# Optimization experiments

Hardware: AMD Instinct MI355X
Metric: run time of the kernel (lower is better)

## Reference

```python
import jax, jax.numpy as jnp
import numpy as np


def setup_inputs() -> dict:
    key0 = jax.random.key(0)
    kq, kk = jax.random.split(key0)
    # query: small template patch; key: larger reference image to search
    query = jax.random.normal(kq, (4, 1, 48, 48), dtype=jnp.float32)
    key = jax.random.normal(kk, (4, 1, 160, 160), dtype=jnp.float32)
    return {"query": query, "key": key}


def reference(query, key):
    B, C, qh, qw = query.shape
    P = key.shape[3] - qw + 1  # static (shape-derived) Python int

    # im2col: extract all overlapping qh x qw patches from key (stride 1, VALID).
    # Output: [B, C*qh*qw, Ho, Wo] with channel ordering (C, kh, kw) -> matches torch unfold.
    patches = jax.lax.conv_general_dilated_patches(
        key, filter_shape=(qh, qw), window_strides=(1, 1), padding='VALID')
    Ho, Wo = patches.shape[2], patches.shape[3]
    L = Ho * Wo
    patches = patches.reshape(B, C, qh * qw, L)  # [B, C, qh*qw, L]

    # Sort pixel values within each patch (dim 2), and within the query patch.
    sorted_key = jnp.sort(patches, axis=2)                       # [B, C, qh*qw, L]
    sorted_query = jnp.sort(query.reshape(B, C, qh * qw, 1), axis=2)  # [B, C, qh*qw, 1]

    # Mean L1 distance between sorted value distributions, reduced over pixels then channels.
    y = jnp.mean(jnp.abs(sorted_key - sorted_query), axis=2)  # [B, C, L]
    y = jnp.mean(y, axis=1)                                   # [B, L]

    hard_indices = jnp.argmin(y, axis=1)  # [B]
    return hard_indices.reshape(-1), P
```

## Files before the change

kernel.cpp:

```cpp
#include <hip/hip_runtime.h>
#include <stdint.h>

#define B_    4
#define QDIM  48
#define KDIM  160
#define HO    113
#define NQ    (QDIM*QDIM)
#define NB    (KDIM*QDIM)
#define NR    (NB+NQ)
#define T_    1024
#define NW    16
#define NP    10
#define NPAD  10240
#define NCH   10
#define NPAIR 57

#define CIDX16(f) ((f) + ((f) >> 4))

__device__ __forceinline__ uint32_t f2s(float v) {
  uint32_t u = __float_as_uint(v);
  return u ^ ((u & 0x80000000u) ? 0xFFFFFFFFu : 0x80000000u);
}
__device__ __forceinline__ float s2f(uint32_t s) {
  return __uint_as_float(s ^ ((s & 0x80000000u) ? 0x80000000u : 0xFFFFFFFFu));
}

__device__ __forceinline__ int dpp_scan_incl(int v) {
  v += __builtin_amdgcn_update_dpp(0, v, 0x111, 0xF, 0xF, false);
  v += __builtin_amdgcn_update_dpp(0, v, 0x112, 0xF, 0xF, false);
  v += __builtin_amdgcn_update_dpp(0, v, 0x114, 0xF, 0xF, false);
  v += __builtin_amdgcn_update_dpp(0, v, 0x118, 0xF, 0xF, false);
  v += __builtin_amdgcn_update_dpp(0, v, 0x142, 0xA, 0xF, false);
  v += __builtin_amdgcn_update_dpp(0, v, 0x143, 0xC, 0xF, false);
  return v;
}

__global__ void ps_init(unsigned long long* slots) {
  if (threadIdx.x < B_) slots[threadIdx.x] = ~0ULL;
}

__global__ __launch_bounds__(T_, 4)
void ps_band_kernel(const float* __restrict__ query,
                    const float* __restrict__ key,
                    unsigned long long* __restrict__ slots) {
  __shared__ unsigned long long E[NPAD];
  __shared__ uint8_t  pA[NPAD];
  __shared__ uint8_t  pB[NPAD];
  alignas(16) __shared__ uint16_t cnt[17408];
  __shared__ int      waveTot[NW], waveBase[NW];
  __shared__ unsigned long long wbest[NW];

  uint32_t* kA = (uint32_t*)E;
  uint32_t* kB = kA + NPAD;

  const int t    = threadIdx.x;
  const int lane = t & 63;
  const int w    = t >> 6;
  const int b    = blockIdx.x / HO;
  const int oy   = blockIdx.x % HO;
  const float* kp = key   + b * KDIM * KDIM;
  const float* qp = query + b * NQ;

  for (int i = t; i < NPAD; i += T_) {
    uint32_t kk, pp;
    if (i < NB) {
      int r = i / KDIM; int x = i - r * KDIM;
      kk = f2s(kp[(oy + r) * KDIM + x]); pp = (uint32_t)x;
    } else if (i < NR) {
      kk = f2s(qp[i - NB]); pp = 255u;
    } else {
      kk = 0xFFFFFFFFu; pp = 254u;
    }
    kA[i] = kk; pA[i] = (uint8_t)pp;
  }
  __syncthreads();

  const int base = t * NP;

  for (int p = 0; p < 8; ++p) {
    uint32_t* sK = (p & 1) ? kB : kA;
    uint32_t* dK = (p & 1) ? kA : kB;
    uint8_t*  sP = (p & 1) ? pB : pA;
    uint8_t*  dP = (p & 1) ? pA : pB;
    const int sh = p * 4;

    for (int i = t; i < 2176; i += T_) ((uint4*)cnt)[i] = make_uint4(0,0,0,0);
    __syncthreads();

    uint32_t kreg[NP]; uint32_t preg[NP];
    {
      const uint2* kv = reinterpret_cast<const uint2*>(sK + base);
      #pragma unroll
      for (int j = 0; j < 5; ++j) { uint2 q = kv[j]; kreg[2*j] = q.x; kreg[2*j+1] = q.y; }
      const uint16_t* pv = reinterpret_cast<const uint16_t*>(sP + base);
      #pragma unroll
      for (int j = 0; j < 5; ++j) { uint32_t q = pv[j]; preg[2*j] = q & 0xFFu; preg[2*j+1] = q >> 8; }
    }

    #pragma unroll
    for (int j = 0; j < NP; ++j) {
      uint32_t f = CIDX16(((kreg[j] >> sh) & 15u) * T_ + t);
      cnt[f] = (uint16_t)(cnt[f] + 1);
    }
    __syncthreads();

    uint32_t cex[16]; int s = 0;
    #pragma unroll
    for (int j = 0; j < 16; ++j) { int c = cnt[CIDX16(16 * t + j)]; cex[j] = (uint32_t)s; s += c; }

    int incl = dpp_scan_incl(s);
    if (lane == 63) waveTot[w] = incl;
    const int wexcl = incl - s;
    __syncthreads();
    if (t < NW) {
      int v = waveTot[t]; int iw = v;
      #pragma unroll
      for (int d = 1; d < NW; d <<= 1) { int o = __shfl_up(iw, d, NW); if (t >= d) iw += o; }
      waveBase[t] = iw - v;
    }
    __syncthreads();
    const int tb = waveBase[w] + wexcl;
    #pragma unroll
    for (int j = 0; j < 16; ++j) cnt[CIDX16(16 * t + j)] = (uint16_t)(cex[j] + (uint32_t)tb);
    __syncthreads();

    #pragma unroll
    for (int j = 0; j < NP; ++j) {
      uint32_t f = CIDX16(((kreg[j] >> sh) & 15u) * T_ + t);
      uint32_t pos = cnt[f];
      cnt[f] = (uint16_t)(pos + 1);
      dK[pos] = kreg[j];
      dP[pos] = (uint8_t)preg[j];
    }
    __syncthreads();
  }

  {
    uint32_t kk2[NP + 1]; uint32_t pp2[NP];
    {
      const uint2* k2 = reinterpret_cast<const uint2*>(kA + base);
      #pragma unroll
      for (int j = 0; j < 5; ++j) { uint2 q = k2[j]; kk2[2*j] = q.x; kk2[2*j+1] = q.y; }
      kk2[NP] = (t == T_ - 1) ? 0xFFFFFFFFu : kA[base + NP];
      const uint16_t* p2 = reinterpret_cast<const uint16_t*>(pA + base);
      #pragma unroll
      for (int j = 0; j < 5; ++j) { uint32_t q = p2[j]; pp2[2*j] = q & 0xFFu; pp2[2*j+1] = q >> 8; }
    }
    __syncthreads();
    #pragma unroll
    for (int j = 0; j < NP; j += 2) {
      int i = base + j;
      float g0 = (i     < NR - 1) ? s2f(kk2[j + 1]) - s2f(kk2[j])     : 0.0f;
      float g1 = (i + 1 < NR - 1) ? s2f(kk2[j + 2]) - s2f(kk2[j + 1]) : 0.0f;
      int c = i >> 10, e = i & 1023;
      int l = e >> 4, sb = (e >> 1) & 7;
      int pidx = c * 1024 + sb * 128 + l * 2;
      E[pidx]     = (unsigned long long)__float_as_uint(g0) | ((unsigned long long)pp2[j]     << 32);
      E[pidx + 1] = (unsigned long long)__float_as_uint(g1) | ((unsigned long long)pp2[j + 1] << 32);
    }
    __syncthreads();
  }

  unsigned long long mybest = ~0ULL;
  for (int pr = w; pr < NPAIR; pr += NW) {
    const int oxa = 2 * pr, oxb = 2 * pr + 1;
    int carry_a = 0, carry_b = 0;
    float acc_a = 0.f, acc_b = 0.f;
    for (int c = 0; c < NCH; ++c) {
      float ga[16]; int pa_[16], pb_[16];
      int ra = 0, rb = 0;
      const uint4* Ep4 = reinterpret_cast<const uint4*>(E + (c * 1024 + lane * 2));
      #pragma unroll
      for (int sb = 0; sb < 8; ++sb) {
        uint4 e = Ep4[sb * 64];
        {
          uint32_t x = e.y;
          int dq = (x == 255u) ? -1 : 0;
          ra += ((x - (uint32_t)oxa) < (uint32_t)QDIM) ? 1 : dq;
          rb += ((x - (uint32_t)oxb) < (uint32_t)QDIM) ? 1 : dq;
          ga[2 * sb] = __uint_as_float(e.x); pa_[2 * sb] = ra; pb_[2 * sb] = rb;
        }
        {
          uint32_t x = e.w;
          int dq = (x == 255u) ? -1 : 0;
          ra += ((x - (uint32_t)oxa) < (uint32_t)QDIM) ? 1 : dq;
          rb += ((x - (uint32_t)oxb) < (uint32_t)QDIM) ? 1 : dq;
          ga[2 * sb + 1] = __uint_as_float(e.z); pa_[2 * sb + 1] = ra; pb_[2 * sb + 1] = rb;
        }
      }
      const int ia = dpp_scan_incl(ra);
      const int ib = dpp_scan_incl(rb);
      const int base_a = carry_a + (ia - ra);
      const int base_b = carry_b + (ib - rb);
      carry_a += __builtin_amdgcn_readlane(ia, 63);
      carry_b += __builtin_amdgcn_readlane(ib, 63);
      #pragma unroll
      for (int j = 0; j < 16; ++j) {
        acc_a = fmaf(fabsf((float)(base_a + pa_[j])), ga[j], acc_a);
        acc_b = fmaf(fabsf((float)(base_b + pb_[j])), ga[j], acc_b);
      }
    }
    #pragma unroll
    for (int d = 32; d >= 1; d >>= 1) {
      acc_a += __shfl_xor(acc_a, d, 64);
      acc_b += __shfl_xor(acc_b, d, 64);
    }
    if (lane == 0) {
      unsigned long long ca =
        (((unsigned long long)__float_as_uint(acc_a)) << 32) | (unsigned)(oy * HO + oxa);
      if (ca < mybest) mybest = ca;
      if (oxb < HO) {
        unsigned long long cb =
          (((unsigned long long)__float_as_uint(acc_b)) << 32) | (unsigned)(oy * HO + oxb);
        if (cb < mybest) mybest = cb;
      }
    }
  }

  if (lane == 0) wbest[w] = mybest;
  __syncthreads();
  if (t == 0) {
    unsigned long long m = wbest[0];
    #pragma unroll
    for (int i = 1; i < NW; ++i) m = (wbest[i] < m) ? wbest[i] : m;
    atomicMin(slots + b, m);
  }
}

__global__ void ps_final(const unsigned long long* __restrict__ slots,
                         int* __restrict__ out) {
  int t = threadIdx.x;
  if (t < B_) out[t] = (int)(unsigned)(slots[t] & 0xFFFFFFFFull);
  if (t == B_) out[t] = HO;
}

extern "C" void kernel_launch(void* const* d_in, const int* in_sizes, int n_in,
                              void* d_out, int out_size, void* d_ws, size_t ws_size,
                              hipStream_t stream) {
  const float* query = (const float*)d_in[0];
  const float* key   = (const float*)d_in[1];
  unsigned long long* slots = (unsigned long long*)d_ws;
  int* out = (int*)d_out;

  hipLaunchKernelGGL(ps_init, dim3(1), dim3(64), 0, stream, slots);
  hipLaunchKernelGGL(ps_band_kernel, dim3(B_ * HO), dim3(T_), 0, stream,
                     query, key, slots);
  hipLaunchKernelGGL(ps_final, dim3(1), dim3(64), 0, stream, slots, out);
}
```

Baseline: 298.5 us.

## Share one radix sort across two adjacent output rows via global staging buffer

A new sort kernel sorts a 49-row band plus the query once per pair of output rows, tagging each value with its band row. It writes two prefix-encoded edge arrays, one per row, to workspace memory. A separate eval kernel loads the matching array and runs the unchanged window scoring, which roughly halves the radix-sort work. The cost is an extra kernel launch, global-memory round trips for about 37 MB of staged data, and 16-bit payload arrays. A fused fallback is kept for when the workspace is too small.

```diff
diff --git a/kernel.cpp b/kernel.cpp
--- a/kernel.cpp
+++ b/kernel.cpp
@@ -8,6 +8,10 @@
 #define NQ    (QDIM*QDIM)
 #define NB    (KDIM*QDIM)
 #define NR    (NB+NQ)
+#define NGRP  57
+#define GROWS 49
+#define NB2   (GROWS*KDIM)
+#define NE2   (NB2+NQ)
 #define T_    1024
 #define NW    16
 #define NP    10
@@ -40,126 +44,156 @@
 }
 
 __global__ __launch_bounds__(T_, 4)
-void ps_band_kernel(const float* __restrict__ query,
+void ps_sort_kernel(const float* __restrict__ query,
                     const float* __restrict__ key,
+                    unsigned long long* __restrict__ Ebase) {
+  __shared__ uint32_t kA[NPAD];
+  __shared__ uint32_t kB[NPAD];
+  __shared__ uint16_t pA[NPAD];
+  __shared__ uint16_t pB[NPAD];
+  alignas(16) __shared__ uint16_t cnt[17408];
+  __shared__ int waveTot[NW], waveBase[NW];
+
+  const int t    = threadIdx.x;
+  const int lane = t & 63;
+  const int w    = t >> 6;
+  const int b    = blockIdx.x / NGRP;
+  const int g    = blockIdx.x % NGRP;
+  const int oy0  = 2 * g;
+  const float* kp = key   + b * KDIM * KDIM;
+  const float* qp = query + b * NQ;
+
+  for (int i = t; i < NPAD; i += T_) {
+    uint32_t kk, pp;
+    if (i < NB2) {
+      int r = i / KDIM, x = i - r * KDIM;
+      int row = oy0 + r;
+      if (row < KDIM) { kk = f2s(kp[row * KDIM + x]); pp = (uint32_t)x | ((uint32_t)r << 8); }
+      else            { kk = 0xFFFFFFFFu; pp = 254u | (63u << 8); }
+    } else if (i < NE2) {
+      kk = f2s(qp[i - NB2]); pp = 255u | (63u << 8) | 0x8000u;
+    } else {
+      kk = 0xFFFFFFFFu; pp = 254u | (63u << 8);
+    }
+    kA[i] = kk; pA[i] = (uint16_t)pp;
+  }
+  __syncthreads();
+
+  const int base = t * NP;
+
+  for (int p = 0; p < 8; ++p) {
+    uint32_t* sK = (p & 1) ? kB : kA;
+    uint32_t* dK = (p & 1) ? kA : kB;
+    uint16_t* sP = (p & 1) ? pB : pA;
+    uint16_t* dP = (p & 1) ? pA : pB;
+    const int sh = p * 4;
+
+    for (int i = t; i < 2176; i += T_) ((uint4*)cnt)[i] = make_uint4(0,0,0,0);
+    __syncthreads();
+
+    uint32_t kreg[NP]; uint32_t preg[NP];
+    {
+      const uint2* kv = reinterpret_cast<const uint2*>(sK + base);
+      #pragma unroll
+      for (int j = 0; j < 5; ++j) { uint2 q = kv[j]; kreg[2*j] = q.x; kreg[2*j+1] = q.y; }
+      const uint32_t* pv = reinterpret_cast<const uint32_t*>(sP + base);
+      #pragma unroll
+      for (int j = 0; j < 5; ++j) { uint32_t q = pv[j]; preg[2*j] = q & 0xFFFFu; preg[2*j+1] = q >> 16; }
+    }
+
+    #pragma unroll
+    for (int j = 0; j < NP; ++j) {
+      uint32_t f = CIDX16(((kreg[j] >> sh) & 15u) * T_ + t);
+      cnt[f] = (uint16_t)(cnt[f] + 1);
+    }
+    __syncthreads();
+
+    uint32_t cex[16]; int s = 0;
+    #pragma unroll
+    for (int j = 0; j < 16; ++j) { int c = cnt[CIDX16(16 * t + j)]; cex[j] = (uint32_t)s; s += c; }
+
+    int incl = dpp_scan_incl(s);
+    if (lane == 63) waveTot[w] = incl;
+    const int wexcl = incl - s;
+    __syncthreads();
+    if (t < NW) {
+      int v = waveTot[t]; int iw = v;
+      #pragma unroll
+      for (int d = 1; d < NW; d <<= 1) { int o = __shfl_up(iw, d, NW); if (t >= d) iw += o; }
+      waveBase[t] = iw - v;
+    }
+    __syncthreads();
+    const int tb = waveBase[w] + wexcl;
+    #pragma unroll
+    for (int j = 0; j < 16; ++j) cnt[CIDX16(16 * t + j)] = (uint16_t)(cex[j] + (uint32_t)tb);
+    __syncthreads();
+
+    #pragma unroll
+    for (int j = 0; j < NP; ++j) {
+      uint32_t f = CIDX16(((kreg[j] >> sh) & 15u) * T_ + t);
+      uint32_t pos = cnt[f];
+      cnt[f] = (uint16_t)(pos + 1);
+      dK[pos] = kreg[j];
+      dP[pos] = (uint16_t)preg[j];
+    }
+    __syncthreads();
+  }
+
+  {
+    uint32_t kk2[NP + 1]; uint32_t pp2[NP];
+    {
+      const uint2* k2 = reinterpret_cast<const uint2*>(kA + base);
+      #pragma unroll
+      for (int j = 0; j < 5; ++j) { uint2 q = k2[j]; kk2[2*j] = q.x; kk2[2*j+1] = q.y; }
+      kk2[NP] = (t == T_ - 1) ? 0xFFFFFFFFu : kA[base + NP];
+      const uint32_t* p2 = reinterpret_cast<const uint32_t*>(pA + base);
+      #pragma unroll
+      for (int j = 0; j < 5; ++j) { uint32_t q = p2[j]; pp2[2*j] = q & 0xFFFFu; pp2[2*j+1] = q >> 16; }
+    }
+    unsigned long long* E0 = Ebase + (size_t)(b * NGRP + g) * 2u * NPAD;
+    unsigned long long* E1 = E0 + NPAD;
+    #pragma unroll
+    for (int j = 0; j < NP; j += 2) {
+      int i = base + j;
+      float g0 = (kk2[j + 1] != 0xFFFFFFFFu) ? s2f(kk2[j + 1]) - s2f(kk2[j])     : 0.0f;
+      float g1 = (kk2[j + 2] != 0xFFFFFFFFu) ? s2f(kk2[j + 2]) - s2f(kk2[j + 1]) : 0.0f;
+      uint32_t x0 = pp2[j] & 255u,   r0 = (pp2[j] >> 8) & 63u,   q0 = pp2[j] >> 15;
+      uint32_t x1 = pp2[j+1] & 255u, r1 = (pp2[j+1] >> 8) & 63u, q1 = pp2[j+1] >> 15;
+      uint32_t a00 = q0 ? 255u : ((r0 < 48u) ? x0 : 254u);
+      uint32_t a01 = q0 ? 255u : (((r0 - 1u) < 48u) ? x0 : 254u);
+      uint32_t a10 = q1 ? 255u : ((r1 < 48u) ? x1 : 254u);
+      uint32_t a11 = q1 ? 255u : (((r1 - 1u) < 48u) ? x1 : 254u);
+      int c = i >> 10, e = i & 1023;
+      int l = e >> 4, sb = (e >> 1) & 7;
+      int pidx = c * 1024 + sb * 128 + l * 2;
+      ulonglong2 v0, v1;
+      v0.x = (unsigned long long)__float_as_uint(g0) | ((unsigned long long)a00 << 32);
+      v0.y = (unsigned long long)__float_as_uint(g1) | ((unsigned long long)a10 << 32);
+      v1.x = (unsigned long long)__float_as_uint(g0) | ((unsigned long long)a01 << 32);
+      v1.y = (unsigned long long)__float_as_uint(g1) | ((unsigned long long)a11 << 32);
+      *reinterpret_cast<ulonglong2*>(E0 + pidx) = v0;
+      *reinterpret_cast<ulonglong2*>(E1 + pidx) = v1;
+    }
+  }
+}
+
+__global__ __launch_bounds__(T_, 4)
+void ps_eval_kernel(const unsigned long long* __restrict__ Ebase,
                     unsigned long long* __restrict__ slots) {
-  __shared__ unsigned long long E[NPAD];
-  __shared__ uint8_t  pA[NPAD];
-  __shared__ uint8_t  pB[NPAD];
-  alignas(16) __shared__ uint16_t cnt[17408];
-  __shared__ int      waveTot[NW], waveBase[NW];
+  __shared__ uint4 E4[NPAD / 2];
   __shared__ unsigned long long wbest[NW];
-
-  uint32_t* kA = (uint32_t*)E;
-  uint32_t* kB = kA + NPAD;
 
   const int t    = threadIdx.x;
   const int lane = t & 63;
   const int w    = t >> 6;
   const int b    = blockIdx.x / HO;
   const int oy   = blockIdx.x % HO;
-  const float* kp = key   + b * KDIM * KDIM;
-  const float* qp = query + b * NQ;
-
-  for (int i = t; i < NPAD; i += T_) {
-    uint32_t kk, pp;
-    if (i < NB) {
-      int r = i / KDIM; int x = i - r * KDIM;
-      kk = f2s(kp[(oy + r) * KDIM + x]); pp = (uint32_t)x;
-    } else if (i < NR) {
-      kk = f2s(qp[i - NB]); pp = 255u;
-    } else {
-      kk = 0xFFFFFFFFu; pp = 254u;
-    }
-    kA[i] = kk; pA[i] = (uint8_t)pp;
-  }
+  const int g    = oy >> 1, sel = oy & 1;
+
+  const uint4* src = reinterpret_cast<const uint4*>(
+      Ebase + ((size_t)(b * NGRP + g) * 2u + (unsigned)sel) * NPAD);
+  for (int i = t; i < NPAD / 2; i += T_) E4[i] = src[i];
   __syncthreads();
-
-  const int base = t * NP;
-
-  for (int p = 0; p < 8; ++p) {
-    uint32_t* sK = (p & 1) ? kB : kA;
-    uint32_t* dK = (p & 1) ? kA : kB;
-    uint8_t*  sP = (p & 1) ? pB : pA;
-    uint8_t*  dP = (p & 1) ? pA : pB;
-    const int sh = p * 4;
-
-    for (int i = t; i < 2176; i += T_) ((uint4*)cnt)[i] = make_uint4(0,0,0,0);
-    __syncthreads();
-
-    uint32_t kreg[NP]; uint32_t preg[NP];
-    {
-      const uint2* kv = reinterpret_cast<const uint2*>(sK + base);
-      #pragma unroll
-      for (int j = 0; j < 5; ++j) { uint2 q = kv[j]; kreg[2*j] = q.x; kreg[2*j+1] = q.y; }
-      const uint16_t* pv = reinterpret_cast<const uint16_t*>(sP + base);
-      #pragma unroll
-      for (int j = 0; j < 5; ++j) { uint32_t q = pv[j]; preg[2*j] = q & 0xFFu; preg[2*j+1] = q >> 8; }
-    }
-
-    #pragma unroll
-    for (int j = 0; j < NP; ++j) {
-      uint32_t f = CIDX16(((kreg[j] >> sh) & 15u) * T_ + t);
-      cnt[f] = (uint16_t)(cnt[f] + 1);
-    }
-    __syncthreads();
-
-    uint32_t cex[16]; int s = 0;
-    #pragma unroll
-    for (int j = 0; j < 16; ++j) { int c = cnt[CIDX16(16 * t + j)]; cex[j] = (uint32_t)s; s += c; }
-
-    int incl = dpp_scan_incl(s);
-    if (lane == 63) waveTot[w] = incl;
-    const int wexcl = incl - s;
-    __syncthreads();
-    if (t < NW) {
-      int v = waveTot[t]; int iw = v;
-      #pragma unroll
-      for (int d = 1; d < NW; d <<= 1) { int o = __shfl_up(iw, d, NW); if (t >= d) iw += o; }
-      waveBase[t] = iw - v;
-    }
-    __syncthreads();
-    const int tb = waveBase[w] + wexcl;
-    #pragma unroll
-    for (int j = 0; j < 16; ++j) cnt[CIDX16(16 * t + j)] = (uint16_t)(cex[j] + (uint32_t)tb);
-    __syncthreads();
-
-    #pragma unroll
-    for (int j = 0; j < NP; ++j) {
-      uint32_t f = CIDX16(((kreg[j] >> sh) & 15u) * T_ + t);
-      uint32_t pos = cnt[f];
-      cnt[f] = (uint16_t)(pos + 1);
-      dK[pos] = kreg[j];
-      dP[pos] = (uint8_t)preg[j];
-    }
-    __syncthreads();
-  }
-
-  {
-    uint32_t kk2[NP + 1]; uint32_t pp2[NP];
-    {
-      const uint2* k2 = reinterpret_cast<const uint2*>(kA + base);
-      #pragma unroll
-      for (int j = 0; j < 5; ++j) { uint2 q = k2[j]; kk2[2*j] = q.x; kk2[2*j+1] = q.y; }
-      kk2[NP] = (t == T_ - 1) ? 0xFFFFFFFFu : kA[base + NP];
-      const uint16_t* p2 = reinterpret_cast<const uint16_t*>(pA + base);
-      #pragma unroll
-      for (int j = 0; j < 5; ++j) { uint32_t q = p2[j]; pp2[2*j] = q & 0xFFu; pp2[2*j+1] = q >> 8; }
-    }
-    __syncthreads();
-    #pragma unroll
-    for (int j = 0; j < NP; j += 2) {
-      int i = base + j;
-      float g0 = (i     < NR - 1) ? s2f(kk2[j + 1]) - s2f(kk2[j])     : 0.0f;
-      float g1 = (i + 1 < NR - 1) ? s2f(kk2[j + 2]) - s2f(kk2[j + 1]) : 0.0f;
-      int c = i >> 10, e = i & 1023;
-      int l = e >> 4, sb = (e >> 1) & 7;
-      int pidx = c * 1024 + sb * 128 + l * 2;
-      E[pidx]     = (unsigned long long)__float_as_uint(g0) | ((unsigned long long)pp2[j]     << 32);
-      E[pidx + 1] = (unsigned long long)__float_as_uint(g1) | ((unsigned long long)pp2[j + 1] << 32);
-    }
-    __syncthreads();
-  }
 
   unsigned long long mybest = ~0ULL;
   for (int pr = w; pr < NPAIR; pr += NW) {
@@ -169,7 +203,7 @@
     for (int c = 0; c < NCH; ++c) {
       float ga[16]; int pa_[16], pb_[16];
       int ra = 0, rb = 0;
-      const uint4* Ep4 = reinterpret_cast<const uint4*>(E + (c * 1024 + lane * 2));
+      const uint4* Ep4 = &E4[c * 512 + lane];
       #pragma unroll
       for (int sb = 0; sb < 8; ++sb) {
         uint4 e = Ep4[sb * 64];
@@ -227,6 +261,194 @@
   }
 }
 
+__global__ __launch_bounds__(T_, 4)
+void ps_band_fused(const float* __restrict__ query,
+                   const float* __restrict__ key,
+                   unsigned long long* __restrict__ slots) {
+  __shared__ unsigned long long E[NPAD];
+  __shared__ uint8_t  pA[NPAD];
+  __shared__ uint8_t  pB[NPAD];
+  alignas(16) __shared__ uint16_t cnt[17408];
+  __shared__ int      waveTot[NW], waveBase[NW];
+  __shared__ unsigned long long wbest[NW];
+
+  uint32_t* kA = (uint32_t*)E;
+  uint32_t* kB = kA + NPAD;
+
+  const int t    = threadIdx.x;
+  const int lane = t & 63;
+  const int w    = t >> 6;
+  const int b    = blockIdx.x / HO;
+  const int oy   = blockIdx.x % HO;
+  const float* kp = key   + b * KDIM * KDIM;
+  const float* qp = query + b * NQ;
+
+  for (int i = t; i < NPAD; i += T_) {
+    uint32_t kk, pp;
+    if (i < NB) {
+      int r = i / KDIM; int x = i - r * KDIM;
+      kk = f2s(kp[(oy + r) * KDIM + x]); pp = (uint32_t)x;
+    } else if (i < NR) {
+      kk = f2s(qp[i - NB]); pp = 255u;
+    } else {
+      kk = 0xFFFFFFFFu; pp = 254u;
+    }
+    kA[i] = kk; pA[i] = (uint8_t)pp;
+  }
+  __syncthreads();
+
+  const int base = t * NP;
+
+  for (int p = 0; p < 8; ++p) {
+    uint32_t* sK = (p & 1) ? kB : kA;
+    uint32_t* dK = (p & 1) ? kA : kB;
+    uint8_t*  sP = (p & 1) ? pB : pA;
+    uint8_t*  dP = (p & 1) ? pA : pB;
+    const int sh = p * 4;
+
+    for (int i = t; i < 2176; i += T_) ((uint4*)cnt)[i] = make_uint4(0,0,0,0);
+    __syncthreads();
+
+    uint32_t kreg[NP]; uint32_t preg[NP];
+    {
+      const uint2* kv = reinterpret_cast<const uint2*>(sK + base);
+      #pragma unroll
+      for (int j = 0; j < 5; ++j) { uint2 q = kv[j]; kreg[2*j] = q.x; kreg[2*j+1] = q.y; }
+      const uint16_t* pv = reinterpret_cast<const uint16_t*>(sP + base);
+      #pragma unroll
+      for (int j = 0; j < 5; ++j) { uint32_t q = pv[j]; preg[2*j] = q & 0xFFu; preg[2*j+1] = q >> 8; }
+    }
+
+    #pragma unroll
+    for (int j = 0; j < NP; ++j) {
+      uint32_t f = CIDX16(((kreg[j] >> sh) & 15u) * T_ + t);
+      cnt[f] = (uint16_t)(cnt[f] + 1);
+    }
+    __syncthreads();
+
+    uint32_t cex[16]; int s = 0;
+    #pragma unroll
+    for (int j = 0; j < 16; ++j) { int c = cnt[CIDX16(16 * t + j)]; cex[j] = (uint32_t)s; s += c; }
+
+    int incl = dpp_scan_incl(s);
+    if (lane == 63) waveTot[w] = incl;
+    const int wexcl = incl - s;
+    __syncthreads();
+    if (t < NW) {
+      int v = waveTot[t]; int iw = v;
+      #pragma unroll
+      for (int d = 1; d < NW; d <<= 1) { int o = __shfl_up(iw, d, NW); if (t >= d) iw += o; }
+      waveBase[t] = iw - v;
+    }
+    __syncthreads();
+    const int tb = waveBase[w] + wexcl;
+    #pragma unroll
+    for (int j = 0; j < 16; ++j) cnt[CIDX16(16 * t + j)] = (uint16_t)(cex[j] + (uint32_t)tb);
+    __syncthreads();
+
+    #pragma unroll
+    for (int j = 0; j < NP; ++j) {
+      uint32_t f = CIDX16(((kreg[j] >> sh) & 15u) * T_ + t);
+      uint32_t pos = cnt[f];
+      cnt[f] = (uint16_t)(pos + 1);
+      dK[pos] = kreg[j];
+      dP[pos] = (uint8_t)preg[j];
+    }
+    __syncthreads();
+  }
+
+  {
+    uint32_t kk2[NP + 1]; uint32_t pp2[NP];
+    {
+      const uint2* k2 = reinterpret_cast<const uint2*>(kA + base);
+      #pragma unroll
+      for (int j = 0; j < 5; ++j) { uint2 q = k2[j]; kk2[2*j] = q.x; kk2[2*j+1] = q.y; }
+      kk2[NP] = (t == T_ - 1) ? 0xFFFFFFFFu : kA[base + NP];
+      const uint16_t* p2 = reinterpret_cast<const uint16_t*>(pA + base);
+      #pragma unroll
+      for (int j = 0; j < 5; ++j) { uint32_t q = p2[j]; pp2[2*j] = q & 0xFFu; pp2[2*j+1] = q >> 8; }
+    }
+    __syncthreads();
+    #pragma unroll
+    for (int j = 0; j < NP; j += 2) {
+      int i = base + j;
+      float g0 = (i     < NR - 1) ? s2f(kk2[j + 1]) - s2f(kk2[j])     : 0.0f;
+      float g1 = (i + 1 < NR - 1) ? s2f(kk2[j + 2]) - s2f(kk2[j + 1]) : 0.0f;
+      int c = i >> 10, e = i & 1023;
+      int l = e >> 4, sb = (e >> 1) & 7;
+      int pidx = c * 1024 + sb * 128 + l * 2;
+      E[pidx]     = (unsigned long long)__float_as_uint(g0) | ((unsigned long long)pp2[j]     << 32);
+      E[pidx + 1] = (unsigned long long)__float_as_uint(g1) | ((unsigned long long)pp2[j + 1] << 32);
+    }
+    __syncthreads();
+  }
+
+  unsigned long long mybest = ~0ULL;
+  for (int pr = w; pr < NPAIR; pr += NW) {
+    const int oxa = 2 * pr, oxb = 2 * pr + 1;
+    int carry_a = 0, carry_b = 0;
+    float acc_a = 0.f, acc_b = 0.f;
+    for (int c = 0; c < NCH; ++c) {
+      float ga[16]; int pa_[16], pb_[16];
+      int ra = 0, rb = 0;
+      const uint4* Ep4 = reinterpret_cast<const uint4*>(E + (c * 1024 + lane * 2));
+      #pragma unroll
+      for (int sb = 0; sb < 8; ++sb) {
+        uint4 e = Ep4[sb * 64];
+        {
+          uint32_t x = e.y;
+          int dq = (x == 255u) ? -1 : 0;
+          ra += ((x - (uint32_t)oxa) < (uint32_t)QDIM) ? 1 : dq;
+          rb += ((x - (uint32_t)oxb) < (uint32_t)QDIM) ? 1 : dq;
+          ga[2 * sb] = __uint_as_float(e.x); pa_[2 * sb] = ra; pb_[2 * sb] = rb;
+        }
+        {
+          uint32_t x = e.w;
+          int dq = (x == 255u) ? -1 : 0;
+          ra += ((x - (uint32_t)oxa) < (uint32_t)QDIM) ? 1 : dq;
+          rb += ((x - (uint32_t)oxb) < (uint32_t)QDIM) ? 1 : dq;
+          ga[2 * sb + 1] = __uint_as_float(e.z); pa_[2 * sb + 1] = ra; pb_[2 * sb + 1] = rb;
+        }
+      }
+      const int ia = dpp_scan_incl(ra);
+      const int ib = dpp_scan_incl(rb);
+      const int base_a = carry_a + (ia - ra);
+      const int base_b = carry_b + (ib - rb);
+      carry_a += __builtin_amdgcn_readlane(ia, 63);
+      carry_b += __builtin_amdgcn_readlane(ib, 63);
+      #pragma unroll
+      for (int j = 0; j < 16; ++j) {
+        acc_a = fmaf(fabsf((float)(base_a + pa_[j])), ga[j], acc_a);
+        acc_b = fmaf(fabsf((float)(base_b + pb_[j])), ga[j], acc_b);
+      }
+    }
+    #pragma unroll
+    for (int d = 32; d >= 1; d >>= 1) {
+      acc_a += __shfl_xor(acc_a, d, 64);
+      acc_b += __shfl_xor(acc_b, d, 64);
+    }
+    if (lane == 0) {
+      unsigned long long ca =
+        (((unsigned long long)__float_as_uint(acc_a)) << 32) | (unsigned)(oy * HO + oxa);
+      if (ca < mybest) mybest = ca;
+      if (oxb < HO) {
+        unsigned long long cb =
+          (((unsigned long long)__float_as_uint(acc_b)) << 32) | (unsigned)(oy * HO + oxb);
+        if (cb < mybest) mybest = cb;
+      }
+    }
+  }
+
+  if (lane == 0) wbest[w] = mybest;
+  __syncthreads();
+  if (t == 0) {
+    unsigned long long m = wbest[0];
+    #pragma unroll
+    for (int i = 1; i < NW; ++i) m = (wbest[i] < m) ? wbest[i] : m;
+    atomicMin(slots + b, m);
+  }
+}
+
 __global__ void ps_final(const unsigned long long* __restrict__ slots,
                          int* __restrict__ out) {
   int t = threadIdx.x;
@@ -242,8 +464,18 @@
   unsigned long long* slots = (unsigned long long*)d_ws;
   int* out = (int*)d_out;
 
+  const size_t need = 256 + (size_t)B_ * NGRP * 2u * NPAD * 8u;
+
   hipLaunchKernelGGL(ps_init, dim3(1), dim3(64), 0, stream, slots);
-  hipLaunchKernelGGL(ps_band_kernel, dim3(B_ * HO), dim3(T_), 0, stream,
-                     query, key, slots);
+  if (ws_size >= need) {
+    unsigned long long* Ebase = (unsigned long long*)((char*)d_ws + 256);
+    hipLaunchKernelGGL(ps_sort_kernel, dim3(B_ * NGRP), dim3(T_), 0, stream,
+                       query, key, Ebase);
+    hipLaunchKernelGGL(ps_eval_kernel, dim3(B_ * HO), dim3(T_), 0, stream,
+                       Ebase, slots);
+  } else {
+    hipLaunchKernelGGL(ps_band_fused, dim3(B_ * HO), dim3(T_), 0, stream,
+                       query, key, slots);
+  }
   hipLaunchKernelGGL(ps_final, dim3(1), dim3(64), 0, stream, slots, out);
 }
```

Result: faster. 270.5 us (-9.4%).
